# Optimization experiments

Measured on AMD Instinct MI355X. Metric: run time of the kernel, lower is better.

Reference implementation:

```python
import jax, jax.numpy as jnp
import numpy as np
import math

H = 16          # num heads
D = 64          # size_per_head
HID = H * D     # 1024
ROT = 32        # rotary_hsize <= D//2


def setup_inputs() -> dict:
    key = jax.random.key(0)
    ks = jax.random.split(key, 10)
    B, S = 2, 2048
    x = jax.random.normal(ks[0], (B, S, HID), dtype=jnp.float32)
    sinusoids = jax.random.normal(ks[1], (B, 2, S, ROT), dtype=jnp.float32)
    attention_bias = jnp.zeros((B, 1, S, S), dtype=jnp.float32)
    scale = 1.0 / math.sqrt(HID)
    Wq = jax.random.normal(ks[2], (HID, HID), dtype=jnp.float32) * scale
    bq = jnp.zeros((HID,), dtype=jnp.float32)
    Wk = jax.random.normal(ks[3], (HID, HID), dtype=jnp.float32) * scale
    bk = jnp.zeros((HID,), dtype=jnp.float32)
    Wv = jax.random.normal(ks[4], (HID, HID), dtype=jnp.float32) * scale
    bv = jnp.zeros((HID,), dtype=jnp.float32)
    Wo = jax.random.normal(ks[5], (HID, HID), dtype=jnp.float32) * scale
    return {"x": x, "sinusoids": sinusoids, "attention_bias": attention_bias,
            "Wq": Wq, "bq": bq, "Wk": Wk, "bk": bk, "Wv": Wv, "bv": bv, "Wo": Wo}


def _apply_rotary(qk, sin, cos):
    # qk: [B,S,H,D]; sin/cos: [B,S,1,ROT]
    r = qk[..., :ROT]
    # stack([-even, odd], -1).reshape -> interleaved (-x0, x1, -x2, x3, ...)
    rt = jnp.stack([-r[..., ::2], r[..., 1::2]], axis=-1).reshape(r.shape)
    return jnp.concatenate([r * cos + rt * sin, qk[..., ROT:]], axis=-1)


def reference(x, sinusoids, attention_bias, Wq, bq, Wk, bk, Wv, bv, Wo):
    B, S, _ = x.shape
    q = (x @ Wq + bq).reshape(B, S, H, D)
    k = (x @ Wk + bk).reshape(B, S, H, D)
    v = (x @ Wv + bv).reshape(B, S, H, D)
    sin = sinusoids[..., 0, :, None, :]  # [B,S,1,ROT]
    cos = sinusoids[..., 1, :, None, :]
    q = _apply_rotary(q, sin, cos)
    k = _apply_rotary(k, sin, cos)
    q = q / math.sqrt(D)
    scores = jnp.einsum('bqhd,bkhd->bhqk', q, k) + attention_bias
    probs = jax.nn.softmax(scores, axis=-1)
    out = jnp.einsum('bhqk,bkhd->bqhd', probs, v).reshape(B, S, HID)
    return out @ Wo
```

## Files before the change

kernel.cpp:

```cpp
#include <hip/hip_runtime.h>
#include <hip/hip_bf16.h>

#define H_   16
#define D_   64
#define HID  1024
#define S_   2048
#define B_   2
#define M_   (B_*S_)
#define ROT  32
#define LOG2E 1.44269504088896341f
#define QSCALE (0.125f * LOG2E)

typedef __bf16 bf16x8 __attribute__((ext_vector_type(8)));
typedef float  f32x4  __attribute__((ext_vector_type(4)));

#define XB_OFF   0u
#define WQT_OFF  (8u<<20)
#define WKT_OFF  (10u<<20)
#define WVT_OFF  (12u<<20)
#define WOT_OFF  (14u<<20)
#define F_OFF    (16u<<20)
#define QH_OFF   ((16u<<20) + (1u<<19))
#define KH_OFF   (QH_OFF + (8u<<20))
#define VT_OFF   (KH_OFF + (8u<<20))
#define AB_OFF   (VT_OFF + (8u<<20))

__device__ __forceinline__ float fexp2(float x) {
#if __has_builtin(__builtin_amdgcn_exp2f)
  return __builtin_amdgcn_exp2f(x);
#else
  return __expf(x * 0.69314718055994531f);
#endif
}

__device__ __forceinline__ unsigned pk2(float a, float b) {
  union { unsigned u; __bf16 h[2]; } w;
  w.h[0] = (__bf16)a; w.h[1] = (__bf16)b;
  return w.u;
}

__global__ __launch_bounds__(256) void prep_kernel(const float* __restrict__ x,
                                                   const float* __restrict__ sinu,
                                                   const float* __restrict__ abias,
                                                   const float* __restrict__ W0, const float* __restrict__ W1,
                                                   const float* __restrict__ W2, const float* __restrict__ W3,
                                                   __hip_bfloat16* __restrict__ xb,
                                                   float* __restrict__ F,
                                                   __hip_bfloat16* __restrict__ T0, __hip_bfloat16* __restrict__ T1,
                                                   __hip_bfloat16* __restrict__ T2, __hip_bfloat16* __restrict__ T3,
                                                   int* __restrict__ flag) {
  __shared__ float tile[32][33];
  int idx = blockIdx.x;
  int tid = threadIdx.x;
  if (idx < 4096) {
    int i = (idx * 256 + tid) * 4;
    float4 v = *(const float4*)(x + i);
    union { __hip_bfloat16 h[4]; uint2 u; } o;
    o.h[0] = __float2bfloat16(v.x);
    o.h[1] = __float2bfloat16(v.y);
    o.h[2] = __float2bfloat16(v.z);
    o.h[3] = __float2bfloat16(v.w);
    *(uint2*)(xb + i) = o.u;
  } else if (idx < 4608) {
    int i = (idx - 4096) * 256 + tid;
    int d  = i & (ROT-1);
    int bs = i >> 5;
    int s  = bs & (S_-1);
    int b  = bs >> 11;
    float sn = sinu[(((size_t)b*2 + 0)*S_ + s)*ROT + d];
    float cs = sinu[(((size_t)b*2 + 1)*S_ + s)*ROT + d];
    F[i] = cs + ((d & 1) ? sn : -sn);
  } else if (idx < 8704) {
    int widx = idx - 4608;
    int z    = widx >> 10;
    int rem  = widx & 1023;
    const float* W = (z==0) ? W0 : (z==1) ? W1 : (z==2) ? W2 : W3;
    __hip_bfloat16* T = (z==0) ? T0 : (z==1) ? T1 : (z==2) ? T2 : T3;
    int bx = (rem & 31) * 32;
    int by = (rem >> 5) * 32;
    int tx = tid & 31, ty = tid >> 5;
    #pragma unroll
    for (int i = 0; i < 4; i++)
      tile[ty + i*8][tx] = W[(size_t)(by + ty + i*8)*HID + bx + tx];
    __syncthreads();
    #pragma unroll
    for (int i = 0; i < 4; i++)
      T[(size_t)(bx + ty + i*8)*HID + by + tx] = __float2bfloat16(tile[tx][ty + i*8]);
  } else {
    size_t i = ((size_t)(idx - 8704) * 256 + tid) * 16;
    const uint4* p = (const uint4*)(abias + i);
    unsigned acc = 0;
    #pragma unroll
    for (int j = 0; j < 4; j++) {
      uint4 u = p[j];
      acc |= u.x | u.y | u.z | u.w;
    }
    if (acc) *flag = 1;
  }
}

__global__ __launch_bounds__(256) void qkv_kernel(const __hip_bfloat16* __restrict__ A,
                                                  const __hip_bfloat16* __restrict__ Bt,
                                                  const float* __restrict__ bq,
                                                  const float* __restrict__ bk,
                                                  const float* __restrict__ bv,
                                                  const float* __restrict__ F,
                                                  __hip_bfloat16* __restrict__ Qh,
                                                  __hip_bfloat16* __restrict__ Kh,
                                                  __hip_bfloat16* __restrict__ Vt) {
  __shared__ __align__(16) __bf16 Asm[2][128*32];
  __shared__ __align__(16) __bf16 Bsm[2][128*32];
  int tid  = threadIdx.x;
  int lane = tid & 63;
  int wv   = tid >> 6;
  int lr   = lane & 15;
  int qd   = lane >> 4;
  int row0 = blockIdx.y * 128;
  int col0 = blockIdx.x * 128;
  int wrow = (wv >> 1) * 64;
  int wcol = (wv & 1) * 64;

  int cg = ((tid & 3) ^ ((tid >> 2) & 3)) * 8;
  const __bf16* Ag = (const __bf16*)A  + (size_t)(row0 + (tid >> 2)) * HID + cg;
  const __bf16* Bg = (const __bf16*)Bt + (size_t)(col0 + (tid >> 2)) * HID + cg;

  f32x4 acc[4][4] = {};

  auto stage = [&](int buf, int k0) {
    __builtin_amdgcn_global_load_lds(Ag + k0,                  &Asm[buf][wv*512],        16, 0, 0);
    __builtin_amdgcn_global_load_lds(Ag + (size_t)64*HID + k0, &Asm[buf][2048 + wv*512], 16, 0, 0);
    __builtin_amdgcn_global_load_lds(Bg + k0,                  &Bsm[buf][wv*512],        16, 0, 0);
    __builtin_amdgcn_global_load_lds(Bg + (size_t)64*HID + k0, &Bsm[buf][2048 + wv*512], 16, 0, 0);
  };

  stage(0, 0);
  int buf = 0;
  for (int k0 = 0; k0 < HID; k0 += 32, buf ^= 1) {
    __syncthreads();
    if (k0 + 32 < HID) stage(buf ^ 1, k0 + 32);
    const __bf16* As = &Asm[buf][0];
    const __bf16* Bs = &Bsm[buf][0];
    bf16x8 a[4], b[4];
    #pragma unroll
    for (int i = 0; i < 4; i++) {
      int row = wrow + i*16 + lr;
      a[i] = *(const bf16x8*)(As + row*32 + ((qd ^ (row & 3)) * 8));
    }
    #pragma unroll
    for (int t = 0; t < 4; t++) {
      int row = wcol + t*16 + lr;
      b[t] = *(const bf16x8*)(Bs + row*32 + ((qd ^ (row & 3)) * 8));
    }
    #pragma unroll
    for (int i = 0; i < 4; i++)
      #pragma unroll
      for (int t = 0; t < 4; t++)
        acc[i][t] = __builtin_amdgcn_mfma_f32_16x16x32_bf16(a[i], b[t], acc[i][t], 0, 0, 0);
  }

  int proj = col0 >> 10;
  int nb   = (col0 & 1023) + wcol;
  const float* bias = (proj == 0) ? bq : ((proj == 1) ? bk : bv);
  #pragma unroll
  for (int i = 0; i < 4; i++) {
    #pragma unroll
    for (int t = 0; t < 4; t++) {
      int nl = nb + t*16 + lr;
      int h  = nl >> 6, d = nl & 63;
      if (proj == 2) {
        int m0 = row0 + wrow + i*16 + qd*4;
        int b2 = m0 >> 11, s0 = m0 & (S_-1);
        union { uint2 u; __bf16 hh[4]; } w;
        #pragma unroll
        for (int r = 0; r < 4; r++)
          w.hh[r] = (__bf16)(acc[i][t][r] + bias[nl]);
        *(uint2*)((__bf16*)Vt + ((size_t)(b2*H_ + h)*D_ + d)*S_ + s0) = w.u;
      } else {
        __hip_bfloat16* dst = (proj == 0) ? Qh : Kh;
        #pragma unroll
        for (int r = 0; r < 4; r++) {
          int m = row0 + wrow + i*16 + qd*4 + r;
          int b2 = m >> 11, s = m & (S_-1);
          float v = acc[i][t][r] + bias[nl];
          if (d < ROT) v *= F[(size_t)(b2*S_ + s)*ROT + d];
          if (proj == 0) v *= QSCALE;
          dst[((size_t)(b2*H_ + h)*S_ + s)*D_ + d] = __float2bfloat16(v);
        }
      }
    }
  }
}

__global__ __launch_bounds__(256) void gemm_o64(const __hip_bfloat16* __restrict__ A,
                                                const __hip_bfloat16* __restrict__ Bt,
                                                float* __restrict__ outf) {
  __shared__ __align__(16) __bf16 Asm[2][128*32];
  __shared__ __align__(16) __bf16 Bsm[2][64*32];
  int tid  = threadIdx.x;
  int lane = tid & 63;
  int wv   = tid >> 6;
  int lr   = lane & 15;
  int qd   = lane >> 4;
  int row0 = blockIdx.y * 128;
  int col0 = blockIdx.x * 64;
  int cg = ((tid & 3) ^ ((tid >> 2) & 3)) * 8;
  const __bf16* Ag = (const __bf16*)A  + (size_t)(row0 + (tid >> 2)) * HID + cg;
  const __bf16* Bg = (const __bf16*)Bt + (size_t)(col0 + (tid >> 2)) * HID + cg;

  f32x4 acc[2][4] = {};
  auto stage = [&](int buf, int k0) {
    __builtin_amdgcn_global_load_lds(Ag + k0,                  &Asm[buf][wv*512],        16, 0, 0);
    __builtin_amdgcn_global_load_lds(Ag + (size_t)64*HID + k0, &Asm[buf][2048 + wv*512], 16, 0, 0);
    __builtin_amdgcn_global_load_lds(Bg + k0,                  &Bsm[buf][wv*512],        16, 0, 0);
  };
  stage(0, 0);
  int buf = 0;
  for (int k0 = 0; k0 < HID; k0 += 32, buf ^= 1) {
    __syncthreads();
    if (k0 + 32 < HID) stage(buf ^ 1, k0 + 32);
    const __bf16* As = &Asm[buf][0];
    const __bf16* Bs = &Bsm[buf][0];
    bf16x8 a[2], b[4];
    #pragma unroll
    for (int i = 0; i < 2; i++) {
      int row = wv*32 + i*16 + lr;
      a[i] = *(const bf16x8*)(As + row*32 + ((qd ^ (row & 3)) * 8));
    }
    #pragma unroll
    for (int t = 0; t < 4; t++) {
      int row = t*16 + lr;
      b[t] = *(const bf16x8*)(Bs + row*32 + ((qd ^ (row & 3)) * 8));
    }
    #pragma unroll
    for (int i = 0; i < 2; i++)
      #pragma unroll
      for (int t = 0; t < 4; t++)
        acc[i][t] = __builtin_amdgcn_mfma_f32_16x16x32_bf16(a[i], b[t], acc[i][t], 0, 0, 0);
  }
  #pragma unroll
  for (int i = 0; i < 2; i++)
    #pragma unroll
    for (int t = 0; t < 4; t++)
      #pragma unroll
      for (int r = 0; r < 4; r++) {
        int m = row0 + wv*32 + i*16 + qd*4 + r;
        int n = col0 + t*16 + lr;
        outf[(size_t)m*HID + n] = acc[i][t][r];
      }
}

#define PSTRIDE 72
__global__ __launch_bounds__(256) void flash_kernel(const __hip_bfloat16* __restrict__ Qh,
                                                    const __hip_bfloat16* __restrict__ Kh,
                                                    const __hip_bfloat16* __restrict__ Vt,
                                                    const float* __restrict__ abias,
                                                    const int* __restrict__ flag,
                                                    __hip_bfloat16* __restrict__ Ab) {
  __shared__ __align__(16) __bf16 Ksm[2][64*64];
  __shared__ __align__(16) __bf16 Vsm[2][64*64];
  __shared__ __align__(16) __bf16 Pb[2][4][32*PSTRIDE];
  int tid  = threadIdx.x;
  int lane = tid & 63;
  int wv   = tid >> 6;
  int lr   = lane & 15;
  int qd   = lane >> 4;
  int idx  = blockIdx.x;
  int xcd  = idx & 7;
  int slot = idx >> 3;
  int bh   = xcd * 4 + (slot >> 4);
  int qblk = slot & 15;
  int b  = bh >> 4;
  int h  = bh & 15;
  int q0 = qblk * 128 + wv * 32;

  const __bf16* Kbase = (const __bf16*)Kh + (size_t)bh*S_*D_;
  const __bf16* Vbase = (const __bf16*)Vt + (size_t)bh*D_*S_;

  const __bf16* Qp = (const __bf16*)Qh + ((size_t)bh*S_ + q0 + lr)*D_ + qd*8;
  bf16x8 qa00 = *(const bf16x8*)(Qp);
  bf16x8 qa01 = *(const bf16x8*)(Qp + 32);
  bf16x8 qa10 = *(const bf16x8*)(Qp + 16*D_);
  bf16x8 qa11 = *(const bf16x8*)(Qp + 16*D_ + 32);

  int hasbias = *flag;
  const float* bp0 = abias + (size_t)b*S_*S_ + (size_t)(q0 + lr)*S_;
  const float* bp1 = bp0 + (size_t)16*S_;

  int rowb = tid >> 3;
  int cg8  = ((tid & 7) ^ (rowb & 7)) * 8;

  auto stageKV = [&](int bf, int kt2) {
    __builtin_amdgcn_global_load_lds(Kbase + (size_t)(kt2 + rowb)*D_ + cg8,      &Ksm[bf][wv*512],        16, 0, 0);
    __builtin_amdgcn_global_load_lds(Kbase + (size_t)(kt2 + 32 + rowb)*D_ + cg8, &Ksm[bf][2048 + wv*512], 16, 0, 0);
    __builtin_amdgcn_global_load_lds(Vbase + (size_t)rowb*S_ + kt2 + cg8,        &Vsm[bf][wv*512],        16, 0, 0);
    __builtin_amdgcn_global_load_lds(Vbase + (size_t)(32 + rowb)*S_ + kt2 + cg8, &Vsm[bf][2048 + wv*512], 16, 0, 0);
  };

  f32x4 oacc0[4] = {}, oacc1[4] = {};
  float lsum0 = 0.f, lsum1 = 0.f;
  bf16x8 vp0[4], vp1[4];
  int sw = lr & 7;

  stageKV(0, 0);
  int buf = 0;
  for (int kt = 0; kt < S_; kt += 64, buf ^= 1) {
    __syncthreads();
    if (kt + 64 < S_) stageKV(buf ^ 1, kt + 64);
    int pcur = (kt >> 6) & 1;
    __bf16* Pc = &Pb[pcur][wv][0];
    const __bf16* Pp = &Pb[pcur ^ 1][wv][0];

    bf16x8 kf0[4], kf1[4];
    #pragma unroll
    for (int c = 0; c < 4; c++) {
      const __bf16* Kr = &Ksm[buf][(c*16 + lr)*64];
      kf0[c] = *(const bf16x8*)(Kr + ((qd       ^ sw) * 8));
      kf1[c] = *(const bf16x8*)(Kr + (((4 + qd) ^ sw) * 8));
    }
    f32x4 s0[4], s1[4];
    #pragma unroll
    for (int c = 0; c < 4; c++) {
      f32x4 z = {};
      z     = __builtin_amdgcn_mfma_f32_16x16x32_bf16(kf0[c], qa00, z, 0, 0, 0);
      s0[c] = __builtin_amdgcn_mfma_f32_16x16x32_bf16(kf1[c], qa01, s0[c] = z, 0, 0, 0);
      f32x4 z2 = {};
      z2    = __builtin_amdgcn_mfma_f32_16x16x32_bf16(kf0[c], qa10, z2, 0, 0, 0);
      s1[c] = __builtin_amdgcn_mfma_f32_16x16x32_bf16(kf1[c], qa11, z2, 0, 0, 0);
    }

    bf16x8 vc0[4], vc1[4];
    #pragma unroll
    for (int t = 0; t < 4; t++) {
      const __bf16* Vr = &Vsm[buf][(t*16 + lr)*64];
      vc0[t] = *(const bf16x8*)(Vr + ((qd       ^ sw) * 8));
      vc1[t] = *(const bf16x8*)(Vr + (((4 + qd) ^ sw) * 8));
    }

    if (kt > 0) {
      bf16x8 pb00 = *(const bf16x8*)(Pp + lr*PSTRIDE + qd*8);
      bf16x8 pb01 = *(const bf16x8*)(Pp + lr*PSTRIDE + 32 + qd*8);
      bf16x8 pb10 = *(const bf16x8*)(Pp + (16+lr)*PSTRIDE + qd*8);
      bf16x8 pb11 = *(const bf16x8*)(Pp + (16+lr)*PSTRIDE + 32 + qd*8);
      #pragma unroll
      for (int t = 0; t < 4; t++) {
        oacc0[t] = __builtin_amdgcn_mfma_f32_16x16x32_bf16(vp0[t], pb00, oacc0[t], 0, 0, 0);
        oacc0[t] = __builtin_amdgcn_mfma_f32_16x16x32_bf16(vp1[t], pb01, oacc0[t], 0, 0, 0);
        oacc1[t] = __builtin_amdgcn_mfma_f32_16x16x32_bf16(vp0[t], pb10, oacc1[t], 0, 0, 0);
        oacc1[t] = __builtin_amdgcn_mfma_f32_16x16x32_bf16(vp1[t], pb11, oacc1[t], 0, 0, 0);
      }
    }

    if (hasbias) {
      #pragma unroll
      for (int c = 0; c < 4; c++) {
        float4 b0 = *(const float4*)(bp0 + kt + c*16 + qd*4);
        float4 b1 = *(const float4*)(bp1 + kt + c*16 + qd*4);
        s0[c][0] += b0.x*LOG2E; s0[c][1] += b0.y*LOG2E; s0[c][2] += b0.z*LOG2E; s0[c][3] += b0.w*LOG2E;
        s1[c][0] += b1.x*LOG2E; s1[c][1] += b1.y*LOG2E; s1[c][2] += b1.z*LOG2E; s1[c][3] += b1.w*LOG2E;
      }
    }
    #pragma unroll
    for (int c = 0; c < 4; c++) {
      float p0 = fexp2(s0[c][0]), p1 = fexp2(s0[c][1]), p2 = fexp2(s0[c][2]), p3 = fexp2(s0[c][3]);
      lsum0 += (p0 + p1) + (p2 + p3);
      *(unsigned*)(Pc + lr*PSTRIDE + c*16 + qd*4)     = pk2(p0, p1);
      *(unsigned*)(Pc + lr*PSTRIDE + c*16 + qd*4 + 2) = pk2(p2, p3);
      float r0 = fexp2(s1[c][0]), r1 = fexp2(s1[c][1]), r2 = fexp2(s1[c][2]), r3 = fexp2(s1[c][3]);
      lsum1 += (r0 + r1) + (r2 + r3);
      *(unsigned*)(Pc + (16+lr)*PSTRIDE + c*16 + qd*4)     = pk2(r0, r1);
      *(unsigned*)(Pc + (16+lr)*PSTRIDE + c*16 + qd*4 + 2) = pk2(r2, r3);
    }

    #pragma unroll
    for (int t = 0; t < 4; t++) { vp0[t] = vc0[t]; vp1[t] = vc1[t]; }
  }

  asm volatile("s_waitcnt lgkmcnt(0)" ::: "memory");
  {
    const __bf16* Pl = &Pb[((S_/64 - 1)) & 1][wv][0];
    bf16x8 pb00 = *(const bf16x8*)(Pl + lr*PSTRIDE + qd*8);
    bf16x8 pb01 = *(const bf16x8*)(Pl + lr*PSTRIDE + 32 + qd*8);
    bf16x8 pb10 = *(const bf16x8*)(Pl + (16+lr)*PSTRIDE + qd*8);
    bf16x8 pb11 = *(const bf16x8*)(Pl + (16+lr)*PSTRIDE + 32 + qd*8);
    #pragma unroll
    for (int t = 0; t < 4; t++) {
      oacc0[t] = __builtin_amdgcn_mfma_f32_16x16x32_bf16(vp0[t], pb00, oacc0[t], 0, 0, 0);
      oacc0[t] = __builtin_amdgcn_mfma_f32_16x16x32_bf16(vp1[t], pb01, oacc0[t], 0, 0, 0);
      oacc1[t] = __builtin_amdgcn_mfma_f32_16x16x32_bf16(vp0[t], pb10, oacc1[t], 0, 0, 0);
      oacc1[t] = __builtin_amdgcn_mfma_f32_16x16x32_bf16(vp1[t], pb11, oacc1[t], 0, 0, 0);
    }
  }

  lsum0 += __shfl_xor(lsum0, 16); lsum0 += __shfl_xor(lsum0, 32);
  lsum1 += __shfl_xor(lsum1, 16); lsum1 += __shfl_xor(lsum1, 32);
  float inv0 = 1.0f / lsum0;
  float inv1 = 1.0f / lsum1;
  size_t ro0 = ((size_t)(b*S_ + q0 + lr))*HID + h*D_;
  size_t ro1 = ((size_t)(b*S_ + q0 + 16 + lr))*HID + h*D_;
  #pragma unroll
  for (int t = 0; t < 4; t++) {
    union { uint2 u; __bf16 hh[4]; } w0, w1;
    #pragma unroll
    for (int r = 0; r < 4; r++) {
      w0.hh[r] = (__bf16)(oacc0[t][r]*inv0);
      w1.hh[r] = (__bf16)(oacc1[t][r]*inv1);
    }
    *(uint2*)((__bf16*)Ab + ro0 + t*16 + qd*4) = w0.u;
    *(uint2*)((__bf16*)Ab + ro1 + t*16 + qd*4) = w1.u;
  }
}

extern "C" void kernel_launch(void* const* d_in, const int* in_sizes, int n_in,
                              void* d_out, int out_size, void* d_ws, size_t ws_size,
                              hipStream_t stream) {
  (void)in_sizes; (void)n_in; (void)out_size; (void)ws_size;
  const float* x     = (const float*)d_in[0];
  const float* sinu  = (const float*)d_in[1];
  const float* abias = (const float*)d_in[2];
  const float* Wq    = (const float*)d_in[3];
  const float* bq    = (const float*)d_in[4];
  const float* Wk    = (const float*)d_in[5];
  const float* bk    = (const float*)d_in[6];
  const float* Wv    = (const float*)d_in[7];
  const float* bv    = (const float*)d_in[8];
  const float* Wo    = (const float*)d_in[9];

  char* ws = (char*)d_ws;
  __hip_bfloat16* Xb  = (__hip_bfloat16*)(ws + XB_OFF);
  __hip_bfloat16* Wqt = (__hip_bfloat16*)(ws + WQT_OFF);
  __hip_bfloat16* Wkt = (__hip_bfloat16*)(ws + WKT_OFF);
  __hip_bfloat16* Wvt = (__hip_bfloat16*)(ws + WVT_OFF);
  __hip_bfloat16* Wot = (__hip_bfloat16*)(ws + WOT_OFF);
  float*          F   = (float*)(ws + F_OFF);
  __hip_bfloat16* Qh  = (__hip_bfloat16*)(ws + QH_OFF);
  __hip_bfloat16* Kh  = (__hip_bfloat16*)(ws + KH_OFF);
  __hip_bfloat16* Vt  = (__hip_bfloat16*)(ws + VT_OFF);
  __hip_bfloat16* Ab  = (__hip_bfloat16*)(ws + AB_OFF);
  int* flag = (int*)d_out;

  hipMemsetAsync(flag, 0, 4, stream);
  prep_kernel<<<10752, 256, 0, stream>>>(x, sinu, abias, Wq, Wk, Wv, Wo,
                                         Xb, F, Wqt, Wkt, Wvt, Wot, flag);

  qkv_kernel<<<dim3(3*HID/128, M_/128), 256, 0, stream>>>(
      Xb, Wqt, bq, bk, bv, F, Qh, Kh, Vt);

  flash_kernel<<<dim3(512), 256, 0, stream>>>(Qh, Kh, Vt, abias, flag, Ab);

  gemm_o64<<<dim3(HID/64, M_/128), 256, 0, stream>>>(Ab, Wot, (float*)d_out);
}
```

Measured before the change: 223.2 us.

## Keep softmax probabilities in registers by permuting V layout, dropping LDS P buffer

The V projection epilogue now writes Vt with a permuted sequence index within each group of 32. This lets the attention kernel feed the exp2 outputs, packed as bf16, directly as MFMA B operands without the round trip through the shared-memory P buffer. The one-iteration software pipeline of the PV product is removed, so PV now uses the current tile's V right after the softmax. s_setprio hints are placed around the MFMA blocks. This saves LDS traffic and space but gives up the overlap the previous pipelining provided.

```diff
diff --git a/kernel.cpp b/kernel.cpp
--- a/kernel.cpp
+++ b/kernel.cpp
@@ -174,7 +174,8 @@
         #pragma unroll
         for (int r = 0; r < 4; r++)
           w.hh[r] = (__bf16)(acc[i][t][r] + bias[nl]);
-        *(uint2*)((__bf16*)Vt + ((size_t)(b2*H_ + h)*D_ + d)*S_ + s0) = w.u;
+        int pos = (s0 & ~31) | ((s0 & 12) << 1) | ((s0 >> 2) & 4);
+        *(uint2*)((__bf16*)Vt + ((size_t)(b2*H_ + h)*D_ + d)*S_ + pos) = w.u;
       } else {
         __hip_bfloat16* dst = (proj == 0) ? Qh : Kh;
         #pragma unroll
@@ -249,7 +250,6 @@
       }
 }
 
-#define PSTRIDE 72
 __global__ __launch_bounds__(256) void flash_kernel(const __hip_bfloat16* __restrict__ Qh,
                                                     const __hip_bfloat16* __restrict__ Kh,
                                                     const __hip_bfloat16* __restrict__ Vt,
@@ -258,7 +258,6 @@
                                                     __hip_bfloat16* __restrict__ Ab) {
   __shared__ __align__(16) __bf16 Ksm[2][64*64];
   __shared__ __align__(16) __bf16 Vsm[2][64*64];
-  __shared__ __align__(16) __bf16 Pb[2][4][32*PSTRIDE];
   int tid  = threadIdx.x;
   int lane = tid & 63;
   int wv   = tid >> 6;
@@ -298,7 +297,6 @@
 
   f32x4 oacc0[4] = {}, oacc1[4] = {};
   float lsum0 = 0.f, lsum1 = 0.f;
-  bf16x8 vp0[4], vp1[4];
   int sw = lr & 7;
 
   stageKV(0, 0);
@@ -306,9 +304,6 @@
   for (int kt = 0; kt < S_; kt += 64, buf ^= 1) {
     __syncthreads();
     if (kt + 64 < S_) stageKV(buf ^ 1, kt + 64);
-    int pcur = (kt >> 6) & 1;
-    __bf16* Pc = &Pb[pcur][wv][0];
-    const __bf16* Pp = &Pb[pcur ^ 1][wv][0];
 
     bf16x8 kf0[4], kf1[4];
     #pragma unroll
@@ -318,37 +313,17 @@
       kf1[c] = *(const bf16x8*)(Kr + (((4 + qd) ^ sw) * 8));
     }
     f32x4 s0[4], s1[4];
+    __builtin_amdgcn_s_setprio(1);
     #pragma unroll
     for (int c = 0; c < 4; c++) {
       f32x4 z = {};
       z     = __builtin_amdgcn_mfma_f32_16x16x32_bf16(kf0[c], qa00, z, 0, 0, 0);
-      s0[c] = __builtin_amdgcn_mfma_f32_16x16x32_bf16(kf1[c], qa01, s0[c] = z, 0, 0, 0);
+      s0[c] = __builtin_amdgcn_mfma_f32_16x16x32_bf16(kf1[c], qa01, z, 0, 0, 0);
       f32x4 z2 = {};
       z2    = __builtin_amdgcn_mfma_f32_16x16x32_bf16(kf0[c], qa10, z2, 0, 0, 0);
       s1[c] = __builtin_amdgcn_mfma_f32_16x16x32_bf16(kf1[c], qa11, z2, 0, 0, 0);
     }
-
-    bf16x8 vc0[4], vc1[4];
-    #pragma unroll
-    for (int t = 0; t < 4; t++) {
-      const __bf16* Vr = &Vsm[buf][(t*16 + lr)*64];
-      vc0[t] = *(const bf16x8*)(Vr + ((qd       ^ sw) * 8));
-      vc1[t] = *(const bf16x8*)(Vr + (((4 + qd) ^ sw) * 8));
-    }
-
-    if (kt > 0) {
-      bf16x8 pb00 = *(const bf16x8*)(Pp + lr*PSTRIDE + qd*8);
-      bf16x8 pb01 = *(const bf16x8*)(Pp + lr*PSTRIDE + 32 + qd*8);
-      bf16x8 pb10 = *(const bf16x8*)(Pp + (16+lr)*PSTRIDE + qd*8);
-      bf16x8 pb11 = *(const bf16x8*)(Pp + (16+lr)*PSTRIDE + 32 + qd*8);
-      #pragma unroll
-      for (int t = 0; t < 4; t++) {
-        oacc0[t] = __builtin_amdgcn_mfma_f32_16x16x32_bf16(vp0[t], pb00, oacc0[t], 0, 0, 0);
-        oacc0[t] = __builtin_amdgcn_mfma_f32_16x16x32_bf16(vp1[t], pb01, oacc0[t], 0, 0, 0);
-        oacc1[t] = __builtin_amdgcn_mfma_f32_16x16x32_bf16(vp0[t], pb10, oacc1[t], 0, 0, 0);
-        oacc1[t] = __builtin_amdgcn_mfma_f32_16x16x32_bf16(vp1[t], pb11, oacc1[t], 0, 0, 0);
-      }
-    }
+    __builtin_amdgcn_s_setprio(0);
 
     if (hasbias) {
       #pragma unroll
@@ -359,36 +334,48 @@
         s1[c][0] += b1.x*LOG2E; s1[c][1] += b1.y*LOG2E; s1[c][2] += b1.z*LOG2E; s1[c][3] += b1.w*LOG2E;
       }
     }
-    #pragma unroll
-    for (int c = 0; c < 4; c++) {
+
+    union { bf16x8 v; unsigned u[4]; } pb00, pb01, pb10, pb11;
+    #pragma unroll
+    for (int c = 0; c < 2; c++) {
       float p0 = fexp2(s0[c][0]), p1 = fexp2(s0[c][1]), p2 = fexp2(s0[c][2]), p3 = fexp2(s0[c][3]);
       lsum0 += (p0 + p1) + (p2 + p3);
-      *(unsigned*)(Pc + lr*PSTRIDE + c*16 + qd*4)     = pk2(p0, p1);
-      *(unsigned*)(Pc + lr*PSTRIDE + c*16 + qd*4 + 2) = pk2(p2, p3);
+      pb00.u[2*c]   = pk2(p0, p1);
+      pb00.u[2*c+1] = pk2(p2, p3);
       float r0 = fexp2(s1[c][0]), r1 = fexp2(s1[c][1]), r2 = fexp2(s1[c][2]), r3 = fexp2(s1[c][3]);
       lsum1 += (r0 + r1) + (r2 + r3);
-      *(unsigned*)(Pc + (16+lr)*PSTRIDE + c*16 + qd*4)     = pk2(r0, r1);
-      *(unsigned*)(Pc + (16+lr)*PSTRIDE + c*16 + qd*4 + 2) = pk2(r2, r3);
-    }
-
-    #pragma unroll
-    for (int t = 0; t < 4; t++) { vp0[t] = vc0[t]; vp1[t] = vc1[t]; }
-  }
-
-  asm volatile("s_waitcnt lgkmcnt(0)" ::: "memory");
-  {
-    const __bf16* Pl = &Pb[((S_/64 - 1)) & 1][wv][0];
-    bf16x8 pb00 = *(const bf16x8*)(Pl + lr*PSTRIDE + qd*8);
-    bf16x8 pb01 = *(const bf16x8*)(Pl + lr*PSTRIDE + 32 + qd*8);
-    bf16x8 pb10 = *(const bf16x8*)(Pl + (16+lr)*PSTRIDE + qd*8);
-    bf16x8 pb11 = *(const bf16x8*)(Pl + (16+lr)*PSTRIDE + 32 + qd*8);
+      pb10.u[2*c]   = pk2(r0, r1);
+      pb10.u[2*c+1] = pk2(r2, r3);
+    }
+    #pragma unroll
+    for (int c = 2; c < 4; c++) {
+      float p0 = fexp2(s0[c][0]), p1 = fexp2(s0[c][1]), p2 = fexp2(s0[c][2]), p3 = fexp2(s0[c][3]);
+      lsum0 += (p0 + p1) + (p2 + p3);
+      pb01.u[2*(c-2)]   = pk2(p0, p1);
+      pb01.u[2*(c-2)+1] = pk2(p2, p3);
+      float r0 = fexp2(s1[c][0]), r1 = fexp2(s1[c][1]), r2 = fexp2(s1[c][2]), r3 = fexp2(s1[c][3]);
+      lsum1 += (r0 + r1) + (r2 + r3);
+      pb11.u[2*(c-2)]   = pk2(r0, r1);
+      pb11.u[2*(c-2)+1] = pk2(r2, r3);
+    }
+
+    bf16x8 vc0[4], vc1[4];
     #pragma unroll
     for (int t = 0; t < 4; t++) {
-      oacc0[t] = __builtin_amdgcn_mfma_f32_16x16x32_bf16(vp0[t], pb00, oacc0[t], 0, 0, 0);
-      oacc0[t] = __builtin_amdgcn_mfma_f32_16x16x32_bf16(vp1[t], pb01, oacc0[t], 0, 0, 0);
-      oacc1[t] = __builtin_amdgcn_mfma_f32_16x16x32_bf16(vp0[t], pb10, oacc1[t], 0, 0, 0);
-      oacc1[t] = __builtin_amdgcn_mfma_f32_16x16x32_bf16(vp1[t], pb11, oacc1[t], 0, 0, 0);
-    }
+      const __bf16* Vr = &Vsm[buf][(t*16 + lr)*64];
+      vc0[t] = *(const bf16x8*)(Vr + ((qd       ^ sw) * 8));
+      vc1[t] = *(const bf16x8*)(Vr + (((4 + qd) ^ sw) * 8));
+    }
+
+    __builtin_amdgcn_s_setprio(1);
+    #pragma unroll
+    for (int t = 0; t < 4; t++) {
+      oacc0[t] = __builtin_amdgcn_mfma_f32_16x16x32_bf16(vc0[t], pb00.v, oacc0[t], 0, 0, 0);
+      oacc0[t] = __builtin_amdgcn_mfma_f32_16x16x32_bf16(vc1[t], pb01.v, oacc0[t], 0, 0, 0);
+      oacc1[t] = __builtin_amdgcn_mfma_f32_16x16x32_bf16(vc0[t], pb10.v, oacc1[t], 0, 0, 0);
+      oacc1[t] = __builtin_amdgcn_mfma_f32_16x16x32_bf16(vc1[t], pb11.v, oacc1[t], 0, 0, 0);
+    }
+    __builtin_amdgcn_s_setprio(0);
   }
 
   lsum0 += __shfl_xor(lsum0, 16); lsum0 += __shfl_xor(lsum0, 32);
```

New measurement: 232.9 us. 1.04x slower.
